# Kernel optimization log

Measured on AMD Instinct MI355X. Metric: run time of the kernel, lower is better.

Reference implementation:

```python
import jax, jax.numpy as jnp
import numpy as np

UNITS = 256
FEAT = 256
NUM_BLOCKS = 4  # start_gru + 2 middle blocks + end_gru
BATCH, T = 128, 384


def _gru_layer(x, kernel, rkernel, bias, return_sequences):
    """Keras GRU (reset_after=True, tanh/sigmoid), zero initial state.
    x: [B,T,D]; kernel: [D,3U]; rkernel: [U,3U]; bias: [2,3U] (input, recurrent).
    Gate order z, r, h as in Keras.
    """
    u = rkernel.shape[0]
    # Precompute input projections for all timesteps (one big GEMM)
    xp = jnp.einsum('btd,dg->btg', x, kernel) + bias[0]  # [B,T,3U]

    def step(h, xt):
        rh = h @ rkernel + bias[1]                 # [B,3U]
        mz, mr, mh = jnp.split(xt, 3, axis=-1)
        rz, rr, rhh = jnp.split(rh, 3, axis=-1)
        z = jax.nn.sigmoid(mz + rz)
        r = jax.nn.sigmoid(mr + rr)
        hh = jnp.tanh(mh + r * rhh)                # reset_after: r applied after recurrent matmul
        h_new = z * h + (1.0 - z) * hh
        return h_new, h_new

    h0 = jnp.zeros((x.shape[0], u), dtype=x.dtype)
    hT, hs = jax.lax.scan(step, h0, jnp.swapaxes(xp, 0, 1))  # scan over time
    return jnp.swapaxes(hs, 0, 1) if return_sequences else hT


def setup_inputs() -> dict:
    key = jax.random.key(0)
    ks = jax.random.split(key, 8)
    s_in = 1.0 / np.sqrt(FEAT)
    s_u = 1.0 / np.sqrt(UNITS)
    x = jax.random.normal(ks[0], (BATCH, T, FEAT), dtype=jnp.float32)
    # first layer params
    k0 = jax.random.normal(ks[1], (FEAT, 3 * UNITS), dtype=jnp.float32) * s_in
    rk0 = jax.random.normal(ks[2], (UNITS, 3 * UNITS), dtype=jnp.float32) * s_u
    b0 = jnp.zeros((2, 3 * UNITS), dtype=jnp.float32)
    # remaining NUM_BLOCKS-1 layers, stacked along leading axis
    L = NUM_BLOCKS - 1
    kern = jax.random.normal(ks[3], (L, UNITS, 3 * UNITS), dtype=jnp.float32) * s_u
    rkern = jax.random.normal(ks[4], (L, UNITS, 3 * UNITS), dtype=jnp.float32) * s_u
    bias = jnp.zeros((L, 2, 3 * UNITS), dtype=jnp.float32)
    return {"x": x, "k0": k0, "rk0": rk0, "b0": b0,
            "kern": kern, "rkern": rkern, "bias": bias}


def reference(x, k0, rk0, b0, kern, rkern, bias):
    # start_gru: return_sequences=True
    h = _gru_layer(x, k0, rk0, b0, return_sequences=True)
    L = kern.shape[0]
    # middle blocks return_sequences=True, last (end_gru) returns final state only
    for i in range(L):
        last = (i == L - 1)
        h = _gru_layer(h, kern[i], rkern[i], bias[i], return_sequences=not last)
    return h  # [B, UNITS]
```

## Files before the change

### kernel.cpp

```cpp
#include <hip/hip_runtime.h>
#include <hip/hip_fp16.h>


#define LAYERS 4
#define TSTEPS 384
#define NCH    8
#define AP2    520
#define WPL    (48 * 16 * 64 * 8)
#define TILE_STRIDE (16 * 64 * 8)
#define RING   16
#define SLOT_ULL (16 * 128)
#define GRP_ULL  (RING * SLOT_ULL)

typedef _Float16 half8 __attribute__((ext_vector_type(8)));
typedef float    f32x4 __attribute__((ext_vector_type(4)));
typedef unsigned long long ull;

#define WP_OFF   0
#define BP_OFF   (LAYERS * WPL * 2)
#define FLAG_OFF (BP_OFF + LAYERS * 1024 * 4)
#define FLAG_BYTES 4096
#define HBUF_OFF (4 * 1024 * 1024)

__global__ void repack_kernel(const float* __restrict__ k0, const float* __restrict__ rk0,
                              const float* __restrict__ b0, const float* __restrict__ kern,
                              const float* __restrict__ rkern, const float* __restrict__ bias,
                              _Float16* __restrict__ Wp, float* __restrict__ Bp)
{
    int idx = blockIdx.x * 256 + threadIdx.x;
    const int total_w = LAYERS * WPL;
    if (idx < total_w) {
        int l = idx / WPL;
        int r = idx - l * WPL;
        int j    = r & 7;
        int lane = (r >> 3) & 63;
        int kt   = (r >> 9) & 15;
        int tile = r >> 13;
        int n = tile * 16 + (lane & 15);
        int k = kt * 32 + (lane >> 4) * 8 + j;
        float v;
        if (l == 0) {
            v = (k < 256) ? k0[(size_t)k * 768 + n] : rk0[(size_t)(k - 256) * 768 + n];
        } else {
            const float* kk = kern  + (size_t)(l - 1) * 256 * 768;
            const float* rk = rkern + (size_t)(l - 1) * 256 * 768;
            v = (k < 256) ? kk[(size_t)k * 768 + n] : rk[(size_t)(k - 256) * 768 + n];
        }
        Wp[idx] = (_Float16)v;
    } else {
        int ib = idx - total_w;
        if (ib < LAYERS * 1024) {
            int l = ib >> 10;
            int i = ib & 1023;
            const float* bs = (l == 0) ? b0 : (bias + (size_t)(l - 1) * 2 * 768);
            float v;
            if (i < 512)      v = bs[i] + bs[768 + i];
            else if (i < 768) v = bs[512 + (i - 512)];
            else              v = bs[768 + 512 + (i - 768)];
            Bp[l * 1024 + i] = v;
        }
    }
}

__launch_bounds__(384, 1)
__global__ void gru_kernel(const float* __restrict__ x,
                           const _Float16* __restrict__ Wp,
                           const float* __restrict__ Bp,
                           ull* __restrict__ hbuf,
                           unsigned int* __restrict__ flags,
                           float* __restrict__ out)
{
    __shared__ _Float16 Ash[16 * AP2];
    __shared__ float    Sc[8][16][17];

    const int tid  = threadIdx.x;
    const int lane = tid & 63;
    const int w    = tid >> 6;
    const int lo16 = lane & 15;
    const int q    = lane >> 4;

    const int s = blockIdx.x & 7;
    const int c = (blockIdx.x >> 3) & 7;
    const int l = blockIdx.x >> 6;
    const int b0row = c * 16;

    const int tile = (w >> 1) * 16 + 2 * s + (w & 1);
    half8 bfrag[16];
    {
        const _Float16* wb = Wp + (size_t)l * WPL + (size_t)tile * TILE_STRIDE;
#pragma unroll
        for (int kt = 0; kt < 16; ++kt)
            bfrag[kt] = *(const half8*)(wb + ((size_t)kt * 64 + lane) * 8);
    }

    const int grow = tid >> 4;
    const int g16  = tid & 15;
    const int gup  = g16 * 2;
    float bz[2] = {0,0}, br[2] = {0,0}, bi[2] = {0,0}, bh[2] = {0,0};
    float hprev[2] = {0.f, 0.f};
    if (tid < 256) {
        const float* bp = Bp + l * 1024;
        int ug = s * 32 + gup;
        bz[0] = bp[ug];       bz[1] = bp[ug + 1];
        br[0] = bp[256 + ug]; br[1] = bp[256 + ug + 1];
        bi[0] = bp[512 + ug]; bi[1] = bp[512 + ug + 1];
        bh[0] = bp[768 + ug]; bh[1] = bp[768 + ug + 1];
    }

    unsigned int* fl_own_g = flags + (l * NCH + c) * 16;
    unsigned int* fl_dn_g  = flags + ((l < 3 ? l + 1 : 0) * NCH + c) * 16;
    unsigned int* my_flag  = fl_own_g + s;

    ull*       hb_own = hbuf + (size_t)(l * NCH + c) * GRP_ULL;
    const ull* hb_up  = hbuf + (size_t)((l > 0 ? l - 1 : 0) * NCH + c) * GRP_ULL;

    auto wait_group = [&](const unsigned int* base, unsigned need) {
        for (;;) {
            unsigned v = 0xFFFFFFFFu;
            if (lane < 8)
                v = __hip_atomic_load(base + lane, __ATOMIC_RELAXED,
                                      __HIP_MEMORY_SCOPE_SYSTEM);
            if (__all((int)(v >= need))) return;
            __builtin_amdgcn_s_sleep(1);
        }
    };

    for (int t = 0; t < TSTEPS; ++t) {
        const int slot  = t & (RING - 1);
        const int pslot = (t - 1) & (RING - 1);
        const bool need_xt = (l > 0);
        const bool need_h  = (t > 0);
        const unsigned xtag = (unsigned)(t + 1);
        const unsigned htag = (unsigned)t;

        ull vx[8], vh[8];
        f32x4 xf0, xf1, xf2, xf3;
        if (tid < 256) {
            const ull* spx = hb_up  + (size_t)slot  * SLOT_ULL + grow * 128 + g16 * 8;
            const ull* sph = hb_own + (size_t)pslot * SLOT_ULL + grow * 128 + g16 * 8;
            if (need_xt) {
#pragma unroll
                for (int j = 0; j < 8; ++j)
                    vx[j] = __hip_atomic_load(spx + j, __ATOMIC_RELAXED, __HIP_MEMORY_SCOPE_SYSTEM);
            } else {
                const float* sp = x + ((size_t)(b0row + grow) * TSTEPS + t) * 256 + gup * 8;
                xf0 = *(const f32x4*)sp;       xf1 = *(const f32x4*)(sp + 4);
                xf2 = *(const f32x4*)(sp + 8); xf3 = *(const f32x4*)(sp + 12);
            }
            if (need_h) {
#pragma unroll
                for (int j = 0; j < 8; ++j)
                    vh[j] = __hip_atomic_load(sph + j, __ATOMIC_RELAXED, __HIP_MEMORY_SCOPE_SYSTEM);
            }
            for (;;) {
                bool ok = true;
                if (need_xt) {
#pragma unroll
                    for (int j = 0; j < 8; ++j)
                        if ((unsigned)(vx[j] >> 32) != xtag) {
                            vx[j] = __hip_atomic_load(spx + j, __ATOMIC_RELAXED, __HIP_MEMORY_SCOPE_SYSTEM);
                            ok = false;
                        }
                }
                if (need_h) {
#pragma unroll
                    for (int j = 0; j < 8; ++j)
                        if ((unsigned)(vh[j] >> 32) != htag) {
                            vh[j] = __hip_atomic_load(sph + j, __ATOMIC_RELAXED, __HIP_MEMORY_SCOPE_SYSTEM);
                            ok = false;
                        }
                }
                if (ok) break;
            }
        }

        if (l < 3 && t >= RING) wait_group(fl_dn_g, (unsigned)(t - RING + 1));

        if (tid < 256) {
            _Float16* arow = Ash + grow * AP2;
            const int eb = g16 * 16;
            if (need_xt) {
#pragma unroll
                for (int j = 0; j < 8; ++j)
                    *(unsigned*)(arow + eb + 2 * j) = (unsigned)vx[j];
            } else {
                half8 h0, h1;
                h0[0]=(_Float16)xf0[0]; h0[1]=(_Float16)xf0[1]; h0[2]=(_Float16)xf0[2]; h0[3]=(_Float16)xf0[3];
                h0[4]=(_Float16)xf1[0]; h0[5]=(_Float16)xf1[1]; h0[6]=(_Float16)xf1[2]; h0[7]=(_Float16)xf1[3];
                h1[0]=(_Float16)xf2[0]; h1[1]=(_Float16)xf2[1]; h1[2]=(_Float16)xf2[2]; h1[3]=(_Float16)xf2[3];
                h1[4]=(_Float16)xf3[0]; h1[5]=(_Float16)xf3[1]; h1[6]=(_Float16)xf3[2]; h1[7]=(_Float16)xf3[3];
                *(half8*)(arow + eb)     = h0;
                *(half8*)(arow + eb + 8) = h1;
            }
            if (need_h) {
#pragma unroll
                for (int j = 0; j < 8; ++j)
                    *(unsigned*)(arow + 256 + eb + 2 * j) = (unsigned)vh[j];
            } else {
#pragma unroll
                for (int j = 0; j < 8; ++j)
                    *(unsigned*)(arow + 256 + eb + 2 * j) = 0u;
            }
        }
        __syncthreads();

        f32x4 acc0 = {0,0,0,0}, acc1 = {0,0,0,0};
#pragma unroll
        for (int kt = 0; kt < 16; ++kt) {
            half8 a = *(const half8*)(Ash + lo16 * AP2 + q * 8 + kt * 32);
            if (w < 4 || kt < 8)
                acc0 = __builtin_amdgcn_mfma_f32_16x16x32_f16(a, bfrag[kt], acc0, 0, 0, 0);
            else
                acc1 = __builtin_amdgcn_mfma_f32_16x16x32_f16(a, bfrag[kt], acc1, 0, 0, 0);
        }
#pragma unroll
        for (int r = 0; r < 4; ++r) Sc[w][q * 4 + r][lo16] = acc0[r];
        if (w >= 4) {
#pragma unroll
            for (int r = 0; r < 4; ++r) Sc[w + 2][q * 4 + r][lo16] = acc1[r];
        }
        __syncthreads();

        if (tid < 256) {
            float hn[2];
#pragma unroll
            for (int j = 0; j < 2; ++j) {
                int u   = gup + j;
                int ut  = u >> 4;
                int col = u & 15;
                float zp = Sc[ut][grow][col]     + bz[j];
                float rp = Sc[2 + ut][grow][col] + br[j];
                float ip = Sc[4 + ut][grow][col] + bi[j];
                float hp = Sc[6 + ut][grow][col] + bh[j];
                float z  = 1.f / (1.f + __expf(-zp));
                float rr = 1.f / (1.f + __expf(-rp));
                float pre = ip + rr * hp;
                float e  = __expf(2.f * pre);
                float th = 1.f - 2.f / (e + 1.f);
                hn[j] = z * hprev[j] + (1.f - z) * th;
                hprev[j] = hn[j];
            }
            union { _Float16 h[2]; unsigned u32; } pk;
            pk.h[0] = (_Float16)hn[0];
            pk.h[1] = (_Float16)hn[1];
            ull word = ((ull)(unsigned)(t + 1) << 32) | (ull)pk.u32;
            __hip_atomic_store(hb_own + (size_t)slot * SLOT_ULL + grow * 128 + s * 16 + g16,
                               word, __ATOMIC_RELAXED, __HIP_MEMORY_SCOPE_SYSTEM);
            if (l == 3 && t == TSTEPS - 1) {
                float* op = out + (size_t)(b0row + grow) * 256 + s * 32 + gup;
                op[0] = hn[0];
                op[1] = hn[1];
            }
        }
        __syncthreads();

        if (tid == 0)
            __hip_atomic_store(my_flag, (unsigned)(t + 1),
                               __ATOMIC_RELAXED, __HIP_MEMORY_SCOPE_SYSTEM);
    }
}

extern "C" void kernel_launch(void* const* d_in, const int* in_sizes, int n_in,
                              void* d_out, int out_size, void* d_ws, size_t ws_size,
                              hipStream_t stream)
{
    const float* x     = (const float*)d_in[0];
    const float* k0    = (const float*)d_in[1];
    const float* rk0   = (const float*)d_in[2];
    const float* b0    = (const float*)d_in[3];
    const float* kern  = (const float*)d_in[4];
    const float* rkern = (const float*)d_in[5];
    const float* bias  = (const float*)d_in[6];
    float* out = (float*)d_out;

    char* ws = (char*)d_ws;
    _Float16*     Wp    = (_Float16*)(ws + WP_OFF);
    float*        Bp    = (float*)(ws + BP_OFF);
    unsigned int* flags = (unsigned int*)(ws + FLAG_OFF);
    ull*          hbuf  = (ull*)(ws + HBUF_OFF);

    hipMemsetAsync(flags, 0, FLAG_BYTES, stream);

    const int total = LAYERS * WPL + LAYERS * 1024;
    repack_kernel<<<(total + 255) / 256, 256, 0, stream>>>(k0, rk0, b0, kern, rkern, bias, Wp, Bp);

    gru_kernel<<<LAYERS * NCH * 8, 384, 0, stream>>>(x, Wp, Bp, hbuf, flags, out);
}
```

Before: 1.752 ms.

## Double-buffer A tile, prefetch next-step input, store in MFMA fragment layout

Adds a two-slot shared A buffer laid out in MFMA fragment order, so each lane reads its A fragment with one contiguous load instead of a padded row layout. The next timestep's input (from the layer below or from x) is staged into the other slot right after the current step's state is written, and the own-hidden-state loads are issued early. This takes upstream input latency off the critical path of the recurrence. The downstream-credit wait now comes after the matmul, and the input poll sleeps between retries. The cost is more shared memory and more complex synchronisation ordering.

```diff
diff --git a/kernel.cpp b/kernel.cpp
--- a/kernel.cpp
+++ b/kernel.cpp
@@ -5,7 +5,6 @@
 #define LAYERS 4
 #define TSTEPS 384
 #define NCH    8
-#define AP2    520
 #define WPL    (48 * 16 * 64 * 8)
 #define TILE_STRIDE (16 * 64 * 8)
 #define RING   16
@@ -14,6 +13,7 @@
 
 typedef _Float16 half8 __attribute__((ext_vector_type(8)));
 typedef float    f32x4 __attribute__((ext_vector_type(4)));
+typedef unsigned uint4v __attribute__((ext_vector_type(4)));
 typedef unsigned long long ull;
 
 #define WP_OFF   0
@@ -70,7 +70,7 @@
                            unsigned int* __restrict__ flags,
                            float* __restrict__ out)
 {
-    __shared__ _Float16 Ash[16 * AP2];
+    __shared__ _Float16 Af[2][16 * 512];
     __shared__ float    Sc[8][16][17];
 
     const int tid  = threadIdx.x;
@@ -96,6 +96,13 @@
     const int grow = tid >> 4;
     const int g16  = tid & 15;
     const int gup  = g16 * 2;
+    const int ktx  = g16 >> 1;
+    const int qq   = (g16 & 1) * 2;
+    const int xoff0 = ((ktx * 64) + qq * 16 + grow) * 8;
+    const int xoff1 = ((ktx * 64) + (qq + 1) * 16 + grow) * 8;
+    const int hoff0 = (((8 + ktx) * 64) + qq * 16 + grow) * 8;
+    const int hoff1 = (((8 + ktx) * 64) + (qq + 1) * 16 + grow) * 8;
+
     float bz[2] = {0,0}, br[2] = {0,0}, bi[2] = {0,0}, bh[2] = {0,0};
     float hprev[2] = {0.f, 0.f};
     if (tid < 256) {
@@ -125,89 +132,82 @@
         }
     };
 
-    for (int t = 0; t < TSTEPS; ++t) {
-        const int slot  = t & (RING - 1);
-        const int pslot = (t - 1) & (RING - 1);
-        const bool need_xt = (l > 0);
-        const bool need_h  = (t > 0);
-        const unsigned xtag = (unsigned)(t + 1);
-        const unsigned htag = (unsigned)t;
-
-        ull vx[8], vh[8];
-        f32x4 xf0, xf1, xf2, xf3;
-        if (tid < 256) {
-            const ull* spx = hb_up  + (size_t)slot  * SLOT_ULL + grow * 128 + g16 * 8;
-            const ull* sph = hb_own + (size_t)pslot * SLOT_ULL + grow * 128 + g16 * 8;
-            if (need_xt) {
-#pragma unroll
-                for (int j = 0; j < 8; ++j)
-                    vx[j] = __hip_atomic_load(spx + j, __ATOMIC_RELAXED, __HIP_MEMORY_SCOPE_SYSTEM);
-            } else {
-                const float* sp = x + ((size_t)(b0row + grow) * TSTEPS + t) * 256 + gup * 8;
-                xf0 = *(const f32x4*)sp;       xf1 = *(const f32x4*)(sp + 4);
-                xf2 = *(const f32x4*)(sp + 8); xf3 = *(const f32x4*)(sp + 12);
-            }
-            if (need_h) {
-#pragma unroll
-                for (int j = 0; j < 8; ++j)
-                    vh[j] = __hip_atomic_load(sph + j, __ATOMIC_RELAXED, __HIP_MEMORY_SCOPE_SYSTEM);
-            }
+    auto stage_x = [&](int t, _Float16* An) {
+        if (l == 0) {
+            const float* sp = x + ((size_t)(b0row + grow) * TSTEPS + t) * 256 + gup * 8;
+            f32x4 a0 = *(const f32x4*)sp,      a1 = *(const f32x4*)(sp + 4);
+            f32x4 a2 = *(const f32x4*)(sp + 8), a3 = *(const f32x4*)(sp + 12);
+            half8 h0, h1;
+            h0[0]=(_Float16)a0[0]; h0[1]=(_Float16)a0[1]; h0[2]=(_Float16)a0[2]; h0[3]=(_Float16)a0[3];
+            h0[4]=(_Float16)a1[0]; h0[5]=(_Float16)a1[1]; h0[6]=(_Float16)a1[2]; h0[7]=(_Float16)a1[3];
+            h1[0]=(_Float16)a2[0]; h1[1]=(_Float16)a2[1]; h1[2]=(_Float16)a2[2]; h1[3]=(_Float16)a2[3];
+            h1[4]=(_Float16)a3[0]; h1[5]=(_Float16)a3[1]; h1[6]=(_Float16)a3[2]; h1[7]=(_Float16)a3[3];
+            *(half8*)(An + xoff0) = h0;
+            *(half8*)(An + xoff1) = h1;
+        } else {
+            const ull* spx = hb_up + (size_t)(t & (RING - 1)) * SLOT_ULL + grow * 128 + g16 * 8;
+            const unsigned tg = (unsigned)(t + 1);
+            ull vx[8];
+#pragma unroll
+            for (int j = 0; j < 8; ++j)
+                vx[j] = __hip_atomic_load(spx + j, __ATOMIC_RELAXED, __HIP_MEMORY_SCOPE_SYSTEM);
             for (;;) {
                 bool ok = true;
-                if (need_xt) {
-#pragma unroll
-                    for (int j = 0; j < 8; ++j)
-                        if ((unsigned)(vx[j] >> 32) != xtag) {
-                            vx[j] = __hip_atomic_load(spx + j, __ATOMIC_RELAXED, __HIP_MEMORY_SCOPE_SYSTEM);
-                            ok = false;
-                        }
-                }
-                if (need_h) {
-#pragma unroll
-                    for (int j = 0; j < 8; ++j)
-                        if ((unsigned)(vh[j] >> 32) != htag) {
-                            vh[j] = __hip_atomic_load(sph + j, __ATOMIC_RELAXED, __HIP_MEMORY_SCOPE_SYSTEM);
-                            ok = false;
-                        }
-                }
+#pragma unroll
+                for (int j = 0; j < 8; ++j)
+                    if ((unsigned)(vx[j] >> 32) != tg) {
+                        vx[j] = __hip_atomic_load(spx + j, __ATOMIC_RELAXED, __HIP_MEMORY_SCOPE_SYSTEM);
+                        ok = false;
+                    }
                 if (ok) break;
-            }
-        }
-
-        if (l < 3 && t >= RING) wait_group(fl_dn_g, (unsigned)(t - RING + 1));
-
-        if (tid < 256) {
-            _Float16* arow = Ash + grow * AP2;
-            const int eb = g16 * 16;
-            if (need_xt) {
+                __builtin_amdgcn_s_sleep(1);
+            }
+            uint4v w0, w1;
+            w0[0]=(unsigned)vx[0]; w0[1]=(unsigned)vx[1]; w0[2]=(unsigned)vx[2]; w0[3]=(unsigned)vx[3];
+            w1[0]=(unsigned)vx[4]; w1[1]=(unsigned)vx[5]; w1[2]=(unsigned)vx[6]; w1[3]=(unsigned)vx[7];
+            *(uint4v*)(An + xoff0) = w0;
+            *(uint4v*)(An + xoff1) = w1;
+        }
+    };
+
+    if (tid < 256) {
+        stage_x(0, Af[0]);
+        uint4v z = {0u, 0u, 0u, 0u};
+        *(uint4v*)(Af[0] + hoff0) = z;
+        *(uint4v*)(Af[0] + hoff1) = z;
+    }
+
+    ull vh[8];
+
+    for (int t = 0; t < TSTEPS; ++t) {
+        _Float16* A  = Af[t & 1];
+        _Float16* An = Af[(t + 1) & 1];
+
+        if (t > 0 && tid < 256) {
+            const ull* sph = hb_own + (size_t)((t - 1) & (RING - 1)) * SLOT_ULL + grow * 128 + g16 * 8;
+            const unsigned tg = (unsigned)t;
+            for (;;) {
+                bool ok = true;
 #pragma unroll
                 for (int j = 0; j < 8; ++j)
-                    *(unsigned*)(arow + eb + 2 * j) = (unsigned)vx[j];
-            } else {
-                half8 h0, h1;
-                h0[0]=(_Float16)xf0[0]; h0[1]=(_Float16)xf0[1]; h0[2]=(_Float16)xf0[2]; h0[3]=(_Float16)xf0[3];
-                h0[4]=(_Float16)xf1[0]; h0[5]=(_Float16)xf1[1]; h0[6]=(_Float16)xf1[2]; h0[7]=(_Float16)xf1[3];
-                h1[0]=(_Float16)xf2[0]; h1[1]=(_Float16)xf2[1]; h1[2]=(_Float16)xf2[2]; h1[3]=(_Float16)xf2[3];
-                h1[4]=(_Float16)xf3[0]; h1[5]=(_Float16)xf3[1]; h1[6]=(_Float16)xf3[2]; h1[7]=(_Float16)xf3[3];
-                *(half8*)(arow + eb)     = h0;
-                *(half8*)(arow + eb + 8) = h1;
-            }
-            if (need_h) {
-#pragma unroll
-                for (int j = 0; j < 8; ++j)
-                    *(unsigned*)(arow + 256 + eb + 2 * j) = (unsigned)vh[j];
-            } else {
-#pragma unroll
-                for (int j = 0; j < 8; ++j)
-                    *(unsigned*)(arow + 256 + eb + 2 * j) = 0u;
-            }
+                    if ((unsigned)(vh[j] >> 32) != tg) {
+                        vh[j] = __hip_atomic_load(sph + j, __ATOMIC_RELAXED, __HIP_MEMORY_SCOPE_SYSTEM);
+                        ok = false;
+                    }
+                if (ok) break;
+            }
+            uint4v w0, w1;
+            w0[0]=(unsigned)vh[0]; w0[1]=(unsigned)vh[1]; w0[2]=(unsigned)vh[2]; w0[3]=(unsigned)vh[3];
+            w1[0]=(unsigned)vh[4]; w1[1]=(unsigned)vh[5]; w1[2]=(unsigned)vh[6]; w1[3]=(unsigned)vh[7];
+            *(uint4v*)(A + hoff0) = w0;
+            *(uint4v*)(A + hoff1) = w1;
         }
         __syncthreads();
 
         f32x4 acc0 = {0,0,0,0}, acc1 = {0,0,0,0};
 #pragma unroll
         for (int kt = 0; kt < 16; ++kt) {
-            half8 a = *(const half8*)(Ash + lo16 * AP2 + q * 8 + kt * 32);
+            half8 a = *(const half8*)(A + ((kt * 64) + lane) * 8);
             if (w < 4 || kt < 8)
                 acc0 = __builtin_amdgcn_mfma_f32_16x16x32_f16(a, bfrag[kt], acc0, 0, 0, 0);
             else
@@ -220,6 +220,8 @@
             for (int r = 0; r < 4; ++r) Sc[w + 2][q * 4 + r][lo16] = acc1[r];
         }
         __syncthreads();
+
+        if (l < 3 && t >= RING) wait_group(fl_dn_g, (unsigned)(t - RING + 1));
 
         if (tid < 256) {
             float hn[2];
@@ -244,13 +246,21 @@
             pk.h[0] = (_Float16)hn[0];
             pk.h[1] = (_Float16)hn[1];
             ull word = ((ull)(unsigned)(t + 1) << 32) | (ull)pk.u32;
-            __hip_atomic_store(hb_own + (size_t)slot * SLOT_ULL + grow * 128 + s * 16 + g16,
+            __hip_atomic_store(hb_own + (size_t)(t & (RING - 1)) * SLOT_ULL + grow * 128 + s * 16 + g16,
                                word, __ATOMIC_RELAXED, __HIP_MEMORY_SCOPE_SYSTEM);
             if (l == 3 && t == TSTEPS - 1) {
                 float* op = out + (size_t)(b0row + grow) * 256 + s * 32 + gup;
                 op[0] = hn[0];
                 op[1] = hn[1];
             }
+        }
+
+        if (t + 1 < TSTEPS && tid < 256) {
+            stage_x(t + 1, An);
+            const ull* sph = hb_own + (size_t)(t & (RING - 1)) * SLOT_ULL + grow * 128 + g16 * 8;
+#pragma unroll
+            for (int j = 0; j < 8; ++j)
+                vh[j] = __hip_atomic_load(sph + j, __ATOMIC_RELAXED, __HIP_MEMORY_SCOPE_SYSTEM);
         }
         __syncthreads();
 
```

New measurement: 1.653 ms. 1.06x faster.
